# Performance work log

Measured on AMD Instinct MI355X. Metric: run time of the kernel, lower is better.

Reference implementation:

```python
import jax, jax.numpy as jnp
import numpy as np

B, N_PER, C, KG, KTOP, KNN = 8, 2048, 256, 16, 512, 32
N = B * N_PER
E = N * KG
EPS = 1e-5


def setup_inputs() -> dict:
    key = jax.random.key(0)
    ks = jax.random.split(key, 32)
    s = 0.05
    x = jax.random.normal(ks[0], (N, C), jnp.float32)
    x_origin = jax.random.normal(ks[1], (N, C), jnp.float32)
    xyz = jax.random.uniform(ks[2], (N, 3), jnp.float32)
    # graph: every node is a dst with KG incoming edges from random nodes of the SAME sample
    edge_dst = jnp.repeat(jnp.arange(N, dtype=jnp.int32), KG)
    src_local = jax.random.randint(ks[3], (E,), 0, N_PER, dtype=jnp.int32)
    edge_src = src_local + (edge_dst // N_PER) * N_PER
    # EdgeConv params (theta on x_j - x_i, phi on x_i)
    theta_w = jax.random.normal(ks[4], (C, C), jnp.float32) * s
    theta_b = jax.random.normal(ks[5], (C,), jnp.float32) * s
    phi_w = jax.random.normal(ks[6], (C, C), jnp.float32) * s
    phi_b = jax.random.normal(ks[7], (C,), jnp.float32) * s
    # region_score_mlp: Conv1d(C,64,1)-ReLU-BN(64)-Conv1d(64,32,1)-ReLU-BN(32)-Conv1d(32,1,1)
    w1 = jax.random.normal(ks[8], (64, C), jnp.float32) * s
    b1 = jax.random.normal(ks[9], (64,), jnp.float32) * s
    g1 = 1.0 + 0.1 * jax.random.normal(ks[10], (64,), jnp.float32)
    be1 = 0.1 * jax.random.normal(ks[11], (64,), jnp.float32)
    m1 = 0.1 * jax.random.normal(ks[12], (64,), jnp.float32)
    v1 = jax.random.uniform(ks[13], (64,), jnp.float32, 0.5, 1.5)
    w2 = jax.random.normal(ks[14], (32, 64), jnp.float32) * s
    b2 = jax.random.normal(ks[15], (32,), jnp.float32) * s
    g2 = 1.0 + 0.1 * jax.random.normal(ks[16], (32,), jnp.float32)
    be2 = 0.1 * jax.random.normal(ks[17], (32,), jnp.float32)
    m2 = 0.1 * jax.random.normal(ks[18], (32,), jnp.float32)
    v2 = jax.random.uniform(ks[19], (32,), jnp.float32, 0.5, 1.5)
    w3 = jax.random.normal(ks[20], (1, 32), jnp.float32) * s
    b3 = jax.random.normal(ks[21], (1,), jnp.float32) * s
    return dict(x=x, x_origin=x_origin, xyz=xyz, edge_src=edge_src, edge_dst=edge_dst,
                theta_w=theta_w, theta_b=theta_b, phi_w=phi_w, phi_b=phi_b,
                w1=w1, b1=b1, g1=g1, be1=be1, m1=m1, v1=v1,
                w2=w2, b2=b2, g2=g2, be2=be2, m2=m2, v2=v2, w3=w3, b3=b3)


def _bn(t, g, b, m, v):
    return (t - m) * jax.lax.rsqrt(v + EPS) * g + b


def _forward(x, x_origin, xyz, edge_src, edge_dst,
             theta_w, theta_b, phi_w, phi_b,
             w1, b1, g1, be1, m1, v1, w2, b2, g2, be2, m2, v2, w3, b3):
    # EdgeConv: h_i = max_{j->i}( theta(x_j - x_i) + phi(x_i) ), then residual add
    msg = ((x[edge_src] - x[edge_dst]) @ theta_w.T + theta_b
           + x[edge_dst] @ phi_w.T + phi_b)                      # [E, C]
    h = jax.ops.segment_max(msg, edge_dst, num_segments=N)       # [N, C]
    x1 = h + x                                                   # residual
    # per-node MLP (Conv1d kernel-size 1 == linear), BN in eval mode
    t = _bn(jax.nn.relu(x1 @ w1.T + b1), g1, be1, m1, v1)
    t = _bn(jax.nn.relu(t @ w2.T + b2), g2, be2, m2, v2)
    score = t @ w3.T + b3                                        # [N, 1]
    score_b = score.reshape(B, N_PER)                            # vps_score
    # per-batch top-k (cls=False path: select by raw score, descending)
    topk_vals, topk_idx = jax.lax.top_k(score_b, KTOP)           # [B, KTOP]
    perm = (topk_idx + jnp.arange(B, dtype=topk_idx.dtype)[:, None] * N_PER).reshape(-1)
    x_new = x1[perm].reshape(B, KTOP, C)
    x_copy = x_origin[perm].reshape(B, KTOP, -1)
    xyz_sel = xyz[perm].reshape(B, KTOP, 3)
    # rebuild 32-NN graph per sample on selected points (batched, no per-b python calls)
    d2 = jnp.sum((xyz_sel[:, :, None, :] - xyz_sel[:, None, :, :]) ** 2, axis=-1)  # [B,K,K]
    _, knn_idx = jax.lax.top_k(-d2, KNN)                         # [B, KTOP, 32]
    return knn_idx, x_new, x_copy, score_b, topk_vals


def reference(x, x_origin, xyz, edge_src, edge_dst,
              theta_w, theta_b, phi_w, phi_b,
              w1, b1, g1, be1, m1, v1, w2, b2, g2, be2, m2, v2, w3, b3):
    return _forward(x, x_origin, xyz, edge_src, edge_dst,
                    theta_w, theta_b, phi_w, phi_b,
                    w1, b1, g1, be1, m1, v1, w2, b2, g2, be2, m2, v2, w3, b3)
```

## Files before the change

### kernel.cpp

```cpp
#include <hip/hip_runtime.h>
#include <math.h>

constexpr int B     = 8;
constexpr int N_PER = 2048;
constexpr int C     = 256;
constexpr int KG    = 16;
constexpr int KTOP  = 512;
constexpr int KNN   = 32;
constexpr int N     = B * N_PER;
constexpr float EPS = 1e-5f;

__global__ __launch_bounds__(256, 2) void k1_dual_gemm(
    const float* __restrict__ x, const float* __restrict__ thw,
    const float* __restrict__ phw, const float* __restrict__ thb,
    const float* __restrict__ phb, float* __restrict__ T, float* __restrict__ R)
{
    constexpr int BK = 16, STX = 132, STW = 68;
    __shared__ float Xs[BK * STX];
    __shared__ float Wt[BK * STW];
    __shared__ float Wp[BK * STW];
    const int tid  = threadIdx.x;
    const int row0 = blockIdx.x * 128;
    const int n0   = blockIdx.y * 64;
    const int tx = tid & 15, ty = tid >> 4;
    const int lm = tid >> 1, lq = (tid & 1) * 8;
    const int wm = tid >> 2, wq = (tid & 3) * 4;

    float aT[8][4] = {{0.f}}, aQ[8][4] = {{0.f}};

    float4 nx0 = *(const float4*)(x   + (size_t)(row0 + lm) * C + lq);
    float4 nx1 = *(const float4*)(x   + (size_t)(row0 + lm) * C + lq + 4);
    float4 nt  = *(const float4*)(thw + (size_t)(n0   + wm) * C + wq);
    float4 np_ = *(const float4*)(phw + (size_t)(n0   + wm) * C + wq);

    for (int k0 = 0; k0 < C; k0 += BK) {
        __syncthreads();
        Xs[(lq + 0) * STX + lm] = nx0.x;  Xs[(lq + 1) * STX + lm] = nx0.y;
        Xs[(lq + 2) * STX + lm] = nx0.z;  Xs[(lq + 3) * STX + lm] = nx0.w;
        Xs[(lq + 4) * STX + lm] = nx1.x;  Xs[(lq + 5) * STX + lm] = nx1.y;
        Xs[(lq + 6) * STX + lm] = nx1.z;  Xs[(lq + 7) * STX + lm] = nx1.w;
        Wt[(wq + 0) * STW + wm] = nt.x;   Wt[(wq + 1) * STW + wm] = nt.y;
        Wt[(wq + 2) * STW + wm] = nt.z;   Wt[(wq + 3) * STW + wm] = nt.w;
        Wp[(wq + 0) * STW + wm] = np_.x;  Wp[(wq + 1) * STW + wm] = np_.y;
        Wp[(wq + 2) * STW + wm] = np_.z;  Wp[(wq + 3) * STW + wm] = np_.w;
        __syncthreads();
        const int kn = k0 + BK;
        if (kn < C) {
            nx0 = *(const float4*)(x   + (size_t)(row0 + lm) * C + kn + lq);
            nx1 = *(const float4*)(x   + (size_t)(row0 + lm) * C + kn + lq + 4);
            nt  = *(const float4*)(thw + (size_t)(n0   + wm) * C + kn + wq);
            np_ = *(const float4*)(phw + (size_t)(n0   + wm) * C + kn + wq);
        }
#pragma unroll
        for (int k = 0; k < BK; ++k) {
            float4 alo = *(const float4*)&Xs[k * STX + ty * 8];
            float4 ahi = *(const float4*)&Xs[k * STX + ty * 8 + 4];
            float4 tv4 = *(const float4*)&Wt[k * STW + tx * 4];
            float4 pv4 = *(const float4*)&Wp[k * STW + tx * 4];
            float av[8] = {alo.x, alo.y, alo.z, alo.w, ahi.x, ahi.y, ahi.z, ahi.w};
            float tv[4] = {tv4.x, tv4.y, tv4.z, tv4.w};
            float pv[4] = {pv4.x, pv4.y, pv4.z, pv4.w};
#pragma unroll
            for (int i2 = 0; i2 < 8; ++i2)
#pragma unroll
                for (int j2 = 0; j2 < 4; ++j2) {
                    aT[i2][j2] += av[i2] * tv[j2];
                    aQ[i2][j2] += av[i2] * pv[j2];
                }
        }
    }

    const int gn = n0 + tx * 4;
    const float4 tb4 = *(const float4*)(thb + gn);
    const float4 pb4 = *(const float4*)(phb + gn);
#pragma unroll
    for (int i2 = 0; i2 < 8; ++i2) {
        const int gm = row0 + ty * 8 + i2;
        const size_t off = (size_t)gm * C + gn;
        float4 xr = *(const float4*)(x + off);
        float4 tvv = make_float4(aT[i2][0], aT[i2][1], aT[i2][2], aT[i2][3]);
        float4 rv;
        rv.x = xr.x + aQ[i2][0] + tb4.x + pb4.x - tvv.x;
        rv.y = xr.y + aQ[i2][1] + tb4.y + pb4.y - tvv.y;
        rv.z = xr.z + aQ[i2][2] + tb4.z + pb4.z - tvv.z;
        rv.w = xr.w + aQ[i2][3] + tb4.w + pb4.w - tvv.w;
        *(float4*)(T + off) = tvv;
        *(float4*)(R + off) = rv;
    }
}

__global__ __launch_bounds__(256) void k2a_gather_max(
    const int* __restrict__ esrc, const float* __restrict__ T, float* x1r)
{
    const int node0 = blockIdx.x * 4;
    const int t = threadIdx.x;
    __shared__ int s[4][KG];
    if (t < 64) s[t >> 4][t & 15] = esrc[(node0 + (t >> 4)) * KG + (t & 15)];
    __syncthreads();
    const int m  = t >> 6;
    const int c4 = (t & 63) * 4;
    float4 acc = make_float4(-INFINITY, -INFINITY, -INFINITY, -INFINITY);
#pragma unroll
    for (int k = 0; k < KG; ++k) {
        const float4 v = *(const float4*)&T[(size_t)s[m][k] * C + c4];
        acc.x = fmaxf(acc.x, v.x);  acc.y = fmaxf(acc.y, v.y);
        acc.z = fmaxf(acc.z, v.z);  acc.w = fmaxf(acc.w, v.w);
    }
    const size_t off = (size_t)(node0 + m) * C + c4;
    float4 r = *(const float4*)&x1r[off];
    r.x += acc.x;  r.y += acc.y;  r.z += acc.z;  r.w += acc.w;
    *(float4*)&x1r[off] = r;
}

__global__ __launch_bounds__(256) void k2bc_score(
    const float* __restrict__ x1, const float* __restrict__ w1,
    const float* __restrict__ b1, const float* __restrict__ g1,
    const float* __restrict__ be1, const float* __restrict__ m1,
    const float* __restrict__ v1,
    const float* __restrict__ w2, const float* __restrict__ b2,
    const float* __restrict__ g2, const float* __restrict__ be2,
    const float* __restrict__ m2, const float* __restrict__ v2,
    const float* __restrict__ w3, const float* __restrict__ b3,
    float* __restrict__ score_ws, float* __restrict__ out_score)
{
    constexpr int BK = 16, ST = 68;
    __shared__ float Xs[BK * ST];
    __shared__ float Ws[BK * ST];
    __shared__ float t1s[64 * 65];
    __shared__ float w2s[32 * 65];
    __shared__ float w3s[32];
    __shared__ float zs[64 * 33];
    const int tid  = threadIdx.x;
    const int row0 = blockIdx.x * 64;
    const int tx = tid & 15, ty = tid >> 4;
    const int lm = tid >> 2, lq = (tid & 3) << 2;

    float acc[4][4] = {{0.f}};
    for (int k0 = 0; k0 < C; k0 += BK) {
        float4 fx = *(const float4*)(x1 + (size_t)(row0 + lm) * C + k0 + lq);
        float4 fw = *(const float4*)(w1 + (size_t)lm * C + k0 + lq);
        __syncthreads();
        Xs[(lq + 0) * ST + lm] = fx.x;  Xs[(lq + 1) * ST + lm] = fx.y;
        Xs[(lq + 2) * ST + lm] = fx.z;  Xs[(lq + 3) * ST + lm] = fx.w;
        Ws[(lq + 0) * ST + lm] = fw.x;  Ws[(lq + 1) * ST + lm] = fw.y;
        Ws[(lq + 2) * ST + lm] = fw.z;  Ws[(lq + 3) * ST + lm] = fw.w;
        __syncthreads();
#pragma unroll
        for (int k = 0; k < BK; ++k) {
            float4 a4 = *(const float4*)&Xs[k * ST + (ty << 2)];
            float4 w4 = *(const float4*)&Ws[k * ST + (tx << 2)];
            float av[4] = {a4.x, a4.y, a4.z, a4.w};
            float wv[4] = {w4.x, w4.y, w4.z, w4.w};
#pragma unroll
            for (int i2 = 0; i2 < 4; ++i2)
#pragma unroll
                for (int j2 = 0; j2 < 4; ++j2) acc[i2][j2] += av[i2] * wv[j2];
        }
    }
    __syncthreads();
#pragma unroll
    for (int i2 = 0; i2 < 4; ++i2) {
        const int mrow = (ty << 2) + i2;
#pragma unroll
        for (int j2 = 0; j2 < 4; ++j2) {
            const int o = (tx << 2) + j2;
            float y = acc[i2][j2] + b1[o];
            y = fmaxf(y, 0.f);
            y = (y - m1[o]) * (1.0f / sqrtf(v1[o] + EPS)) * g1[o] + be1[o];
            t1s[mrow * 65 + o] = y;
        }
    }
    for (int idx = tid; idx < 2048; idx += 256)
        w2s[(idx >> 6) * 65 + (idx & 63)] = w2[idx];
    if (tid < 32) w3s[tid] = w3[tid];
    __syncthreads();

    const int o = tid & 31;
    const float inv2 = (1.0f / sqrtf(v2[o] + EPS)) * g2[o];
#pragma unroll
    for (int p = 0; p < 8; ++p) {
        const int nl = p * 8 + (tid >> 5);
        float z = 0.f;
#pragma unroll
        for (int j = 0; j < 64; ++j) z += t1s[nl * 65 + j] * w2s[o * 65 + j];
        z += b2[o];
        z = fmaxf(z, 0.f);
        z = (z - m2[o]) * inv2 + be2[o];
        zs[nl * 33 + o] = z;
    }
    __syncthreads();

    if (tid < 64) {
        float sacc = 0.f;
#pragma unroll
        for (int j = 0; j < 32; ++j) sacc += zs[tid * 33 + j] * w3s[j];
        sacc += b3[0];
        const int node = row0 + tid;
        score_ws[node]  = sacc;
        out_score[node] = sacc;
    }
}

__global__ __launch_bounds__(1024) void k3_topk(
    const float* __restrict__ score, float* __restrict__ out_topk,
    int* __restrict__ perm)
{
    __shared__ unsigned long long keys[N_PER];
    const int b = blockIdx.x;
    const int t = threadIdx.x;
    for (int i = t; i < N_PER; i += 1024) {
        const float v = score[b * N_PER + i];
        unsigned u = __float_as_uint(v);
        const unsigned ua = (u & 0x80000000u) ? ~u : (u | 0x80000000u);
        const unsigned ud = ~ua;
        keys[i] = ((unsigned long long)ud << 32) | (unsigned)i;
    }
    __syncthreads();
    for (int k = 2; k <= N_PER; k <<= 1) {
        for (int j = k >> 1; j > 0; j >>= 1) {
            for (int i = t; i < N_PER; i += 1024) {
                const int ixj = i ^ j;
                if (ixj > i) {
                    const unsigned long long a = keys[i], c = keys[ixj];
                    const bool up = ((i & k) == 0);
                    if ((a > c) == up) { keys[i] = c; keys[ixj] = a; }
                }
            }
            __syncthreads();
        }
    }
    for (int r = t; r < KTOP; r += 1024) {
        const int idx = (int)(keys[r] & 0xffffffffu);
        out_topk[b * KTOP + r] = score[b * N_PER + idx];
        perm[b * KTOP + r] = b * N_PER + idx;
    }
}

__global__ __launch_bounds__(256) void k5_knn(
    const int* __restrict__ perm, const float* __restrict__ xyz,
    const float* __restrict__ x1, const float* __restrict__ xorig,
    float* __restrict__ out_xnew, float* __restrict__ out_xcopy,
    float* __restrict__ out_knn)
{
    constexpr int G = 4;
    __shared__ float px[KTOP], py[KTOP], pz[KTOP];
    __shared__ unsigned long long keys[G * KTOP];
    const int t  = threadIdx.x;
    const int q0 = blockIdx.x * G;
    const int b  = q0 >> 9;
    const int i0 = q0 & 511;

    for (int idx = t; idx < KTOP; idx += 256) {
        const int g = perm[b * KTOP + idx];
        px[idx] = xyz[g * 3 + 0];
        py[idx] = xyz[g * 3 + 1];
        pz[idx] = xyz[g * 3 + 2];
    }
#pragma unroll
    for (int p = 0; p < G; ++p) {
        const int row = q0 + p;
        const int g = perm[row];
        out_xnew [(size_t)row * C + t] = x1   [(size_t)g * C + t];
        out_xcopy[(size_t)row * C + t] = xorig[(size_t)g * C + t];
    }
    __syncthreads();

    for (int w = t; w < G * KTOP; w += 256) {
        const int p = w >> 9, idx = w & 511;
        const float dx = __fsub_rn(px[i0 + p], px[idx]);
        const float dy = __fsub_rn(py[i0 + p], py[idx]);
        const float dz = __fsub_rn(pz[i0 + p], pz[idx]);
        const float d2 = __fadd_rn(__fadd_rn(__fmul_rn(dx, dx), __fmul_rn(dy, dy)),
                                   __fmul_rn(dz, dz));
        keys[w] = ((unsigned long long)__float_as_uint(d2) << 32) | (unsigned)idx;
    }
    __syncthreads();

    for (int k = 2; k <= 32; k <<= 1) {
        for (int j = k >> 1; j > 0; j >>= 1) {
            for (int i = t; i < G * KTOP; i += 256) {
                const int ixj = i ^ j;
                if (ixj > i) {
                    const int il = i & 31;
                    const unsigned long long a = keys[i], c = keys[ixj];
                    const bool up = ((il & k) == 0) || (k == 32);
                    if ((a > c) == up) { keys[i] = c; keys[ixj] = a; }
                }
            }
            __syncthreads();
        }
    }
    for (int r = 0; r < 4; ++r) {
        const int npairs = 8 >> r;
        const int total  = G * npairs * 32;
        for (int w = t; w < total; w += 256) {
            const int p  = w / (npairs * 32);
            const int rm = w - p * (npairs * 32);
            const int m  = rm >> 5, i = rm & 31;
            const int baseA = p * KTOP + m * (64 << r);
            const int baseB = baseA + (32 << r);
            const unsigned long long a = keys[baseA + i];
            const unsigned long long c = keys[baseB + 31 - i];
            keys[baseA + i] = (c < a) ? c : a;
        }
        __syncthreads();
        for (int j = 16; j > 0; j >>= 1) {
            for (int w = t; w < total; w += 256) {
                const int p  = w / (npairs * 32);
                const int rm = w - p * (npairs * 32);
                const int m  = rm >> 5, i = rm & 31;
                const int ixj = i ^ j;
                if (ixj > i) {
                    const int baseA = p * KTOP + m * (64 << r);
                    const unsigned long long a = keys[baseA + i], c = keys[baseA + ixj];
                    if (a > c) { keys[baseA + i] = c; keys[baseA + ixj] = a; }
                }
            }
            __syncthreads();
        }
    }

    if (t < G * KNN) {
        const int p = t >> 5, r = t & 31;
        out_knn[((size_t)(q0 + p)) * KNN + r] =
            (float)(unsigned)(keys[p * KTOP + r] & 0xffffffffu);
    }
}

extern "C" void kernel_launch(void* const* d_in, const int* in_sizes, int n_in,
                              void* d_out, int out_size, void* d_ws, size_t ws_size,
                              hipStream_t stream)
{
    const float* x     = (const float*)d_in[0];
    const float* xorig = (const float*)d_in[1];
    const float* xyz   = (const float*)d_in[2];
    const int*   esrc  = (const int*)d_in[3];
    const float* thw = (const float*)d_in[5];
    const float* thb = (const float*)d_in[6];
    const float* phw = (const float*)d_in[7];
    const float* phb = (const float*)d_in[8];
    const float* w1  = (const float*)d_in[9];
    const float* b1  = (const float*)d_in[10];
    const float* g1  = (const float*)d_in[11];
    const float* be1 = (const float*)d_in[12];
    const float* m1  = (const float*)d_in[13];
    const float* v1  = (const float*)d_in[14];
    const float* w2  = (const float*)d_in[15];
    const float* b2  = (const float*)d_in[16];
    const float* g2  = (const float*)d_in[17];
    const float* be2 = (const float*)d_in[18];
    const float* m2  = (const float*)d_in[19];
    const float* v2  = (const float*)d_in[20];
    const float* w3  = (const float*)d_in[21];
    const float* b3  = (const float*)d_in[22];

    float* ws   = (float*)d_ws;
    float* T    = ws;
    float* x1   = ws + (size_t)N * C;
    float* sc   = ws + 2 * (size_t)N * C;
    int*   perm = (int*)(sc + N);

    float* out     = (float*)d_out;
    float* o_knn   = out;
    float* o_xnew  = o_knn + (size_t)B * KTOP * KNN;
    float* o_xcopy = o_xnew + (size_t)B * KTOP * C;
    float* o_score = o_xcopy + (size_t)B * KTOP * C;
    float* o_topk  = o_score + (size_t)B * N_PER;

    k1_dual_gemm<<<dim3(N / 128, C / 64), 256, 0, stream>>>(x, thw, phw, thb, phb, T, x1);
    k2a_gather_max<<<N / 4, 256, 0, stream>>>(esrc, T, x1);
    k2bc_score<<<N / 64, 256, 0, stream>>>(x1, w1, b1, g1, be1, m1, v1,
                                           w2, b2, g2, be2, m2, v2, w3, b3, sc, o_score);
    k3_topk<<<B, 1024, 0, stream>>>(sc, o_topk, perm);
    k5_knn<<<B * KTOP / 4, 256, 0, stream>>>(perm, xyz, x1, xorig,
                                             o_xnew, o_xcopy, o_knn);
}
```

Baseline: 276.9 us.

## Double-buffer dual GEMM smem and stage per-sample T channels in LDS for gather-max

The dual GEMM now uses two shared-memory buffers, so the next K tile is written while the current one is consumed, saving one barrier per iteration. The gather-max kernel is restructured so each block owns one sample and four channels. It loads that sample's 2048x4 slice of T into LDS and does the 16-way neighbor max from LDS rather than from scattered global float4 loads. This relies on edges staying within their own sample, which the input construction guarantees. The trade-offs are narrow 4-float strided global reads when loading T, scalar output writes, and only 512 blocks with large LDS use.

```diff
diff --git a/kernel.cpp b/kernel.cpp
--- a/kernel.cpp
+++ b/kernel.cpp
@@ -16,9 +16,9 @@
     const float* __restrict__ phb, float* __restrict__ T, float* __restrict__ R)
 {
     constexpr int BK = 16, STX = 132, STW = 68;
-    __shared__ float Xs[BK * STX];
-    __shared__ float Wt[BK * STW];
-    __shared__ float Wp[BK * STW];
+    __shared__ float Xs[2][BK * STX];
+    __shared__ float Wt[2][BK * STW];
+    __shared__ float Wp[2][BK * STW];
     const int tid  = threadIdx.x;
     const int row0 = blockIdx.x * 128;
     const int n0   = blockIdx.y * 64;
@@ -32,18 +32,18 @@
     float4 nx1 = *(const float4*)(x   + (size_t)(row0 + lm) * C + lq + 4);
     float4 nt  = *(const float4*)(thw + (size_t)(n0   + wm) * C + wq);
     float4 np_ = *(const float4*)(phw + (size_t)(n0   + wm) * C + wq);
-
+    Xs[0][(lq + 0) * STX + lm] = nx0.x;  Xs[0][(lq + 1) * STX + lm] = nx0.y;
+    Xs[0][(lq + 2) * STX + lm] = nx0.z;  Xs[0][(lq + 3) * STX + lm] = nx0.w;
+    Xs[0][(lq + 4) * STX + lm] = nx1.x;  Xs[0][(lq + 5) * STX + lm] = nx1.y;
+    Xs[0][(lq + 6) * STX + lm] = nx1.z;  Xs[0][(lq + 7) * STX + lm] = nx1.w;
+    Wt[0][(wq + 0) * STW + wm] = nt.x;   Wt[0][(wq + 1) * STW + wm] = nt.y;
+    Wt[0][(wq + 2) * STW + wm] = nt.z;   Wt[0][(wq + 3) * STW + wm] = nt.w;
+    Wp[0][(wq + 0) * STW + wm] = np_.x;  Wp[0][(wq + 1) * STW + wm] = np_.y;
+    Wp[0][(wq + 2) * STW + wm] = np_.z;  Wp[0][(wq + 3) * STW + wm] = np_.w;
+    __syncthreads();
+
+    int p = 0;
     for (int k0 = 0; k0 < C; k0 += BK) {
-        __syncthreads();
-        Xs[(lq + 0) * STX + lm] = nx0.x;  Xs[(lq + 1) * STX + lm] = nx0.y;
-        Xs[(lq + 2) * STX + lm] = nx0.z;  Xs[(lq + 3) * STX + lm] = nx0.w;
-        Xs[(lq + 4) * STX + lm] = nx1.x;  Xs[(lq + 5) * STX + lm] = nx1.y;
-        Xs[(lq + 6) * STX + lm] = nx1.z;  Xs[(lq + 7) * STX + lm] = nx1.w;
-        Wt[(wq + 0) * STW + wm] = nt.x;   Wt[(wq + 1) * STW + wm] = nt.y;
-        Wt[(wq + 2) * STW + wm] = nt.z;   Wt[(wq + 3) * STW + wm] = nt.w;
-        Wp[(wq + 0) * STW + wm] = np_.x;  Wp[(wq + 1) * STW + wm] = np_.y;
-        Wp[(wq + 2) * STW + wm] = np_.z;  Wp[(wq + 3) * STW + wm] = np_.w;
-        __syncthreads();
         const int kn = k0 + BK;
         if (kn < C) {
             nx0 = *(const float4*)(x   + (size_t)(row0 + lm) * C + kn + lq);
@@ -51,12 +51,15 @@
             nt  = *(const float4*)(thw + (size_t)(n0   + wm) * C + kn + wq);
             np_ = *(const float4*)(phw + (size_t)(n0   + wm) * C + kn + wq);
         }
+        const float* Xp = Xs[p];
+        const float* Tp = Wt[p];
+        const float* Pp = Wp[p];
 #pragma unroll
         for (int k = 0; k < BK; ++k) {
-            float4 alo = *(const float4*)&Xs[k * STX + ty * 8];
-            float4 ahi = *(const float4*)&Xs[k * STX + ty * 8 + 4];
-            float4 tv4 = *(const float4*)&Wt[k * STW + tx * 4];
-            float4 pv4 = *(const float4*)&Wp[k * STW + tx * 4];
+            float4 alo = *(const float4*)&Xp[k * STX + ty * 8];
+            float4 ahi = *(const float4*)&Xp[k * STX + ty * 8 + 4];
+            float4 tv4 = *(const float4*)&Tp[k * STW + tx * 4];
+            float4 pv4 = *(const float4*)&Pp[k * STW + tx * 4];
             float av[8] = {alo.x, alo.y, alo.z, alo.w, ahi.x, ahi.y, ahi.z, ahi.w};
             float tv[4] = {tv4.x, tv4.y, tv4.z, tv4.w};
             float pv[4] = {pv4.x, pv4.y, pv4.z, pv4.w};
@@ -68,6 +71,19 @@
                     aQ[i2][j2] += av[i2] * pv[j2];
                 }
         }
+        if (kn < C) {
+            const int q = p ^ 1;
+            Xs[q][(lq + 0) * STX + lm] = nx0.x;  Xs[q][(lq + 1) * STX + lm] = nx0.y;
+            Xs[q][(lq + 2) * STX + lm] = nx0.z;  Xs[q][(lq + 3) * STX + lm] = nx0.w;
+            Xs[q][(lq + 4) * STX + lm] = nx1.x;  Xs[q][(lq + 5) * STX + lm] = nx1.y;
+            Xs[q][(lq + 6) * STX + lm] = nx1.z;  Xs[q][(lq + 7) * STX + lm] = nx1.w;
+            Wt[q][(wq + 0) * STW + wm] = nt.x;   Wt[q][(wq + 1) * STW + wm] = nt.y;
+            Wt[q][(wq + 2) * STW + wm] = nt.z;   Wt[q][(wq + 3) * STW + wm] = nt.w;
+            Wp[q][(wq + 0) * STW + wm] = np_.x;  Wp[q][(wq + 1) * STW + wm] = np_.y;
+            Wp[q][(wq + 2) * STW + wm] = np_.z;  Wp[q][(wq + 3) * STW + wm] = np_.w;
+            __syncthreads();
+        }
+        p ^= 1;
     }
 
     const int gn = n0 + tx * 4;
@@ -92,24 +108,39 @@
 __global__ __launch_bounds__(256) void k2a_gather_max(
     const int* __restrict__ esrc, const float* __restrict__ T, float* x1r)
 {
-    const int node0 = blockIdx.x * 4;
-    const int t = threadIdx.x;
-    __shared__ int s[4][KG];
-    if (t < 64) s[t >> 4][t & 15] = esrc[(node0 + (t >> 4)) * KG + (t & 15)];
-    __syncthreads();
-    const int m  = t >> 6;
-    const int c4 = (t & 63) * 4;
-    float4 acc = make_float4(-INFINITY, -INFINITY, -INFINITY, -INFINITY);
-#pragma unroll
-    for (int k = 0; k < KG; ++k) {
-        const float4 v = *(const float4*)&T[(size_t)s[m][k] * C + c4];
-        acc.x = fmaxf(acc.x, v.x);  acc.y = fmaxf(acc.y, v.y);
-        acc.z = fmaxf(acc.z, v.z);  acc.w = fmaxf(acc.w, v.w);
-    }
-    const size_t off = (size_t)(node0 + m) * C + c4;
-    float4 r = *(const float4*)&x1r[off];
-    r.x += acc.x;  r.y += acc.y;  r.z += acc.z;  r.w += acc.w;
-    *(float4*)&x1r[off] = r;
+    constexpr int CH = 4, TST = 5, DTILE = 64;
+    __shared__ float Ts[N_PER * TST];
+    __shared__ int   sidx[DTILE * 17];
+    const int b  = blockIdx.y;
+    const int c0 = blockIdx.x * CH;
+    const int t  = threadIdx.x;
+
+    {
+        const int ch = t & 3;
+        for (int r = t >> 2; r < N_PER; r += 64)
+            Ts[r * TST + ch] = T[((size_t)(b * N_PER + r)) * C + c0 + ch];
+    }
+    __syncthreads();
+
+    const int chv = t & 3;
+    const int dl  = t >> 2;
+    for (int d0 = 0; d0 < N_PER; d0 += DTILE) {
+        const int4 e4 = *(const int4*)&esrc[((size_t)(b * N_PER + d0)) * KG + t * 4];
+        const int dd = t >> 2, kk = (t & 3) * 4;
+        sidx[dd * 17 + kk + 0] = e4.x;  sidx[dd * 17 + kk + 1] = e4.y;
+        sidx[dd * 17 + kk + 2] = e4.z;  sidx[dd * 17 + kk + 3] = e4.w;
+        __syncthreads();
+
+        float m = -INFINITY;
+#pragma unroll
+        for (int k = 0; k < KG; ++k) {
+            const int s = sidx[dl * 17 + k] - b * N_PER;
+            m = fmaxf(m, Ts[s * TST + chv]);
+        }
+        const size_t off = ((size_t)(b * N_PER + d0 + dl)) * C + c0 + chv;
+        x1r[off] = m + x1r[off];
+        __syncthreads();
+    }
 }
 
 __global__ __launch_bounds__(256) void k2bc_score(
@@ -368,7 +399,7 @@
     float* o_topk  = o_score + (size_t)B * N_PER;
 
     k1_dual_gemm<<<dim3(N / 128, C / 64), 256, 0, stream>>>(x, thw, phw, thb, phb, T, x1);
-    k2a_gather_max<<<N / 4, 256, 0, stream>>>(esrc, T, x1);
+    k2a_gather_max<<<dim3(C / 4, B), 256, 0, stream>>>(esrc, T, x1);
     k2bc_score<<<N / 64, 256, 0, stream>>>(x1, w1, b1, g1, be1, m1, v1,
                                            w2, b2, g2, be2, m2, v2, w3, b3, sc, o_score);
     k3_topk<<<B, 1024, 0, stream>>>(sc, o_topk, perm);
```

Result: slower. 317.4 us (+14.6%).
